# Kernel tuning notes

Measured on AMD Instinct MI355X. Metric: run time of the kernel, lower is better.

The kernel has to match this reference:

```python
import jax, jax.numpy as jnp
import numpy as np

LN_EPS = 1e-5  # torch nn.LayerNorm default

def _layer_norm(x, w, b):
    m = jnp.mean(x, axis=-1, keepdims=True)
    v = jnp.mean(jnp.square(x - m), axis=-1, keepdims=True)
    return (x - m) * jax.lax.rsqrt(v + LN_EPS) * w + b

def setup_inputs() -> dict:
    R, N, D, A = 8, 8192, 2048, 128
    init_scale = 0.01
    key = jax.random.key(0)
    k0, k1, k2 = jax.random.split(key, 3)
    x = jax.random.normal(k0, (N, D), jnp.float32)
    ln_w = jnp.ones((R, D), jnp.float32)              # per-router input LayerNorm weight
    ln_b = jnp.zeros((R, D), jnp.float32)
    router_weights = jax.random.normal(k1, (R, D, A), jnp.float32) * init_scale
    rw_ln_w = jax.random.normal(k2, (R, D), jnp.float32) * init_scale  # weight-LN gamma (init ones*scale in src)
    rw_ln_b = jnp.zeros((R, D), jnp.float32)
    router_bias = jnp.zeros((R, A), jnp.float32)
    return {"x": x, "ln_w": ln_w, "ln_b": ln_b, "router_weights": router_weights,
            "rw_ln_w": rw_ln_w, "rw_ln_b": rw_ln_b, "router_bias": router_bias}

def reference(x, ln_w, ln_b, router_weights, rw_ln_w, rw_ln_b, router_bias):
    # Per-router LayerNorm of shared input x: new_x [R, N, D]
    new_x = jax.vmap(lambda w, b: _layer_norm(x, w, b))(ln_w, ln_b)
    # normalize_router_weights=True: LayerNorm over in_dim of W[i].T, then transpose back
    rw_norm = jax.vmap(lambda W, w, b: _layer_norm(W.T, w, b).T)(router_weights, rw_ln_w, rw_ln_b)  # [R, D, A]
    adapter_logits = jnp.einsum('rnd,rda->rna', new_x, rw_norm) + router_bias[:, None, :]
    adapter_probs = jax.nn.softmax(adapter_logits, axis=-1)
    return new_x, adapter_logits, adapter_probs
```

## Files before the change

kernel.cpp:

```cpp
#include <hip/hip_runtime.h>
#include <hip/hip_bf16.h>
#include <stdint.h>

#define R_ 8
#define N_ 8192
#define D_ 2048
#define A_ 128
#define J_ 1024
#define LN_EPS 1e-5f

typedef __attribute__((ext_vector_type(8))) short bf16x8;
typedef __attribute__((ext_vector_type(4))) float f32x4;

__device__ inline ushort f2bf(float f) {
    union { float f; uint32_t u; } v; v.f = f;
    uint32_t u = v.u;
    return (ushort)((u + 0x7fffu + ((u >> 16) & 1u)) >> 16);
}
__device__ inline float bf2f(ushort u) {
    union { uint32_t u; float f; } v; v.u = ((uint32_t)u) << 16;
    return v.f;
}

__global__ __launch_bounds__(256) void k_prep(
    const float* __restrict__ x,
    const float* __restrict__ W,
    const float* __restrict__ ln_w,
    const float* __restrict__ ln_b,
    const float* __restrict__ rw_w,
    const float* __restrict__ rw_b,
    const float* __restrict__ rbias,
    ushort* __restrict__ xhat,
    ushort* __restrict__ Bt,
    float* __restrict__ cvec)
{
    __shared__ float sm[16];
    const int t = threadIdx.x;

    if (blockIdx.x < N_) {
        const int n = blockIdx.x;
        const float* xr = x + (size_t)n * D_;
        float4 v0 = *(const float4*)(xr + t * 4);
        float4 v1 = *(const float4*)(xr + 1024 + t * 4);
        float s  = v0.x + v0.y + v0.z + v0.w + v1.x + v1.y + v1.z + v1.w;
        float sq = v0.x*v0.x + v0.y*v0.y + v0.z*v0.z + v0.w*v0.w
                 + v1.x*v1.x + v1.y*v1.y + v1.z*v1.z + v1.w*v1.w;
        #pragma unroll
        for (int o = 32; o > 0; o >>= 1) {
            s  += __shfl_xor(s,  o, 64);
            sq += __shfl_xor(sq, o, 64);
        }
        if ((t & 63) == 0) { sm[t >> 6] = s; sm[8 + (t >> 6)] = sq; }
        __syncthreads();
        s  = sm[0] + sm[1] + sm[2] + sm[3];
        sq = sm[8] + sm[9] + sm[10] + sm[11];
        const float mean = s * (1.0f / D_);
        const float var  = sq * (1.0f / D_) - mean * mean;
        const float rstd = rsqrtf(var + LN_EPS);

        ushort4 p0 = make_ushort4(f2bf((v0.x - mean) * rstd), f2bf((v0.y - mean) * rstd),
                                  f2bf((v0.z - mean) * rstd), f2bf((v0.w - mean) * rstd));
        ushort4 p1 = make_ushort4(f2bf((v1.x - mean) * rstd), f2bf((v1.y - mean) * rstd),
                                  f2bf((v1.z - mean) * rstd), f2bf((v1.w - mean) * rstd));
        *(ushort4*)(xhat + (size_t)n * D_ + t * 4)        = p0;
        *(ushort4*)(xhat + (size_t)n * D_ + 1024 + t * 4) = p1;
    } else {
        const int j = blockIdx.x - N_;
        const int r = j >> 7, a = j & 127;
        const float* Wc = W + (size_t)r * D_ * A_ + a;

        float vals[8];
        float s = 0.f, sq = 0.f;
        #pragma unroll
        for (int k = 0; k < 8; ++k) {
            float v = Wc[(size_t)(t + k * 256) * A_];
            vals[k] = v; s += v; sq += v * v;
        }
        #pragma unroll
        for (int o = 32; o > 0; o >>= 1) {
            s  += __shfl_xor(s,  o, 64);
            sq += __shfl_xor(sq, o, 64);
        }
        if ((t & 63) == 0) { sm[t >> 6] = s; sm[8 + (t >> 6)] = sq; }
        __syncthreads();
        s  = sm[0] + sm[1] + sm[2] + sm[3];
        sq = sm[8] + sm[9] + sm[10] + sm[11];
        const float mean = s * (1.0f / D_);
        const float var  = sq * (1.0f / D_) - mean * mean;
        const float rstd = rsqrtf(var + LN_EPS);

        float cp = 0.f;
        #pragma unroll
        for (int k = 0; k < 8; ++k) {
            const int d = t + k * 256;
            const float nv = (vals[k] - mean) * rstd * rw_w[(size_t)r * D_ + d]
                           + rw_b[(size_t)r * D_ + d];
            Bt[(size_t)j * D_ + d] = f2bf(ln_w[(size_t)r * D_ + d] * nv);
            cp += ln_b[(size_t)r * D_ + d] * nv;
        }
        __syncthreads();
        #pragma unroll
        for (int o = 32; o > 0; o >>= 1) cp += __shfl_xor(cp, o, 64);
        if ((t & 63) == 0) sm[t >> 6] = cp;
        __syncthreads();
        if (t == 0) cvec[j] = sm[0] + sm[1] + sm[2] + sm[3] + rbias[(size_t)r * A_ + a];
    }
}

__global__ __launch_bounds__(256) void k_fused(
    const ushort* __restrict__ Xh,
    const ushort* __restrict__ Bt,
    const float* __restrict__ cvec,
    const float* __restrict__ ln_w,
    const float* __restrict__ ln_b,
    float* __restrict__ new_x,
    float* __restrict__ logits,
    float* __restrict__ probs)
{
    __shared__ __attribute__((aligned(16))) ushort As[64 * 32];
    __shared__ __attribute__((aligned(16))) ushort Bs[128 * 32];
    __shared__ __attribute__((aligned(16))) float lwS[D_];
    __shared__ __attribute__((aligned(16))) float lbS[D_];

    const int t    = threadIdx.x;
    const int lane = t & 63;
    const int w    = t >> 6;
    const int r    = blockIdx.x & 7;
    const int mt   = blockIdx.x >> 3;
    const int m0   = mt * 64;
    const int j0   = r * 128;

    #pragma unroll
    for (int i = 0; i < 2; ++i) {
        const int idx = t + i * 256;
        ((float4*)lwS)[idx] = ((const float4*)(ln_w + (size_t)r * D_))[idx];
        ((float4*)lbS)[idx] = ((const float4*)(ln_b + (size_t)r * D_))[idx];
    }

    f32x4 acc[8];
    #pragma unroll
    for (int jf = 0; jf < 8; ++jf) acc[jf] = (f32x4){0.f, 0.f, 0.f, 0.f};

    float* nx_base = new_x + ((size_t)r * N_ + m0) * D_;

    for (int kt = 0; kt < D_ / 32; ++kt) {
        __syncthreads();
        {
            const int row = t >> 2;
            const int kc  = t & 3;
            const ushort* gA = Xh + (size_t)(m0 + row) * D_ + kt * 32 + kc * 8;
            __builtin_amdgcn_global_load_lds(
                (const __attribute__((address_space(1))) void*)gA,
                (__attribute__((address_space(3))) void*)(&As[t * 8]), 16, 0, 0);
        }
        #pragma unroll
        for (int c = 0; c < 2; ++c) {
            const int q   = t + c * 256;
            const int row = q >> 2;
            const int kc  = q & 3;
            const ushort* gB = Bt + (size_t)(j0 + row) * D_ + kt * 32 + kc * 8;
            __builtin_amdgcn_global_load_lds(
                (const __attribute__((address_space(1))) void*)gB,
                (__attribute__((address_space(3))) void*)(&Bs[q * 8]), 16, 0, 0);
        }
        __syncthreads();

        const int kbase = kt * 32;
        #pragma unroll
        for (int c = 0; c < 2; ++c) {
            const int q    = t + c * 256;
            const int row  = q >> 3;
            const int col4 = q & 7;
            const int d    = kbase + col4 * 4;
            const ushort4 hb = *(const ushort4*)(&As[row * 32 + col4 * 4]);
            const float4 lw4 = *(const float4*)(&lwS[d]);
            const float4 lb4 = *(const float4*)(&lbS[d]);
            f32x4 o;
            o[0] = bf2f(hb.x) * lw4.x + lb4.x;
            o[1] = bf2f(hb.y) * lw4.y + lb4.y;
            o[2] = bf2f(hb.z) * lw4.z + lb4.z;
            o[3] = bf2f(hb.w) * lw4.w + lb4.w;
            __builtin_nontemporal_store(o, (f32x4*)(nx_base + (size_t)row * D_ + d));
        }

        const bf16x8 afr = *(const bf16x8*)(&As[(w * 16 + (lane & 15)) * 32
                                                + (lane >> 4) * 8]);
        #pragma unroll
        for (int jf = 0; jf < 8; ++jf) {
            const bf16x8 bfr = *(const bf16x8*)(&Bs[(jf * 16 + (lane & 15)) * 32
                                                    + (lane >> 4) * 8]);
            acc[jf] = __builtin_amdgcn_mfma_f32_16x16x32_bf16(afr, bfr, acc[jf], 0, 0, 0);
        }
    }

    float cv[8];
    #pragma unroll
    for (int jf = 0; jf < 8; ++jf) cv[jf] = cvec[j0 + jf * 16 + (lane & 15)];

    #pragma unroll
    for (int reg = 0; reg < 4; ++reg) {
        const int row = m0 + w * 16 + (lane >> 4) * 4 + reg;
        float v[8], e[8];
        float mx = -3.4e38f;
        #pragma unroll
        for (int jf = 0; jf < 8; ++jf) {
            v[jf] = acc[jf][reg] + cv[jf];
            mx = fmaxf(mx, v[jf]);
        }
        #pragma unroll
        for (int o = 8; o > 0; o >>= 1) mx = fmaxf(mx, __shfl_xor(mx, o, 64));
        float ssum = 0.f;
        #pragma unroll
        for (int jf = 0; jf < 8; ++jf) { e[jf] = __expf(v[jf] - mx); ssum += e[jf]; }
        #pragma unroll
        for (int o = 8; o > 0; o >>= 1) ssum += __shfl_xor(ssum, o, 64);
        const float inv = 1.0f / ssum;
        float* lrow = logits + ((size_t)r * N_ + row) * A_;
        float* prow = probs  + ((size_t)r * N_ + row) * A_;
        #pragma unroll
        for (int jf = 0; jf < 8; ++jf) {
            const int aa = jf * 16 + (lane & 15);
            __builtin_nontemporal_store(v[jf], lrow + aa);
            __builtin_nontemporal_store(e[jf] * inv, prow + aa);
        }
    }
}

extern "C" void kernel_launch(void* const* d_in, const int* in_sizes, int n_in,
                              void* d_out, int out_size, void* d_ws, size_t ws_size,
                              hipStream_t stream)
{
    const float* x     = (const float*)d_in[0];
    const float* ln_w  = (const float*)d_in[1];
    const float* ln_b  = (const float*)d_in[2];
    const float* W     = (const float*)d_in[3];
    const float* rw_w  = (const float*)d_in[4];
    const float* rw_b  = (const float*)d_in[5];
    const float* rbias = (const float*)d_in[6];

    float* out    = (float*)d_out;
    float* new_x  = out;
    float* logits = out + (size_t)R_ * N_ * D_;
    float* probs  = logits + (size_t)R_ * N_ * A_;

    ushort* xhat = (ushort*)d_ws;
    ushort* Btp  = (ushort*)((char*)d_ws + (size_t)N_ * D_ * 2);
    float*  cvec = (float*)((char*)d_ws + (size_t)N_ * D_ * 2 + (size_t)J_ * D_ * 2);

    hipLaunchKernelGGL(k_prep, dim3(N_ + J_), dim3(256), 0, stream,
                       x, W, ln_w, ln_b, rw_w, rw_b, rbias, xhat, Btp, cvec);
    hipLaunchKernelGGL(k_fused, dim3(J_), dim3(256), 0, stream,
                       xhat, Btp, cvec, ln_w, ln_b, new_x, logits, probs);
}
```

Baseline: 191.3 us.

## Double K tile to 64 with XOR-swizzled LDS and bf16 LayerNorm params

Doubles the K step of the fused GEMM loop from 32 to 64, which halves the number of barrier-separated load phases. The A and B tiles are now stored in LDS with an XOR swizzle on the 16-byte chunk index to reduce bank conflicts on the MFMA fragment reads and on the new_x epilogue reads. The per-router LayerNorm weight and bias are kept in LDS as bf16 instead of fp32 to save shared memory. In exchange, new_x loses some precision for arbitrary ln_w/ln_b values, and the larger tiles raise register and LDS pressure per block.

```diff
diff --git a/kernel.cpp b/kernel.cpp
--- a/kernel.cpp
+++ b/kernel.cpp
@@ -117,10 +117,10 @@
     float* __restrict__ logits,
     float* __restrict__ probs)
 {
-    __shared__ __attribute__((aligned(16))) ushort As[64 * 32];
-    __shared__ __attribute__((aligned(16))) ushort Bs[128 * 32];
-    __shared__ __attribute__((aligned(16))) float lwS[D_];
-    __shared__ __attribute__((aligned(16))) float lbS[D_];
+    __shared__ __attribute__((aligned(16))) ushort As[64 * 64];
+    __shared__ __attribute__((aligned(16))) ushort Bs[128 * 64];
+    __shared__ __attribute__((aligned(16))) ushort lwS[D_];
+    __shared__ __attribute__((aligned(16))) ushort lbS[D_];
 
     const int t    = threadIdx.x;
     const int lane = t & 63;
@@ -130,11 +130,15 @@
     const int m0   = mt * 64;
     const int j0   = r * 128;
 
-    #pragma unroll
-    for (int i = 0; i < 2; ++i) {
-        const int idx = t + i * 256;
-        ((float4*)lwS)[idx] = ((const float4*)(ln_w + (size_t)r * D_))[idx];
-        ((float4*)lbS)[idx] = ((const float4*)(ln_b + (size_t)r * D_))[idx];
+    {
+        const float4 wa = ((const float4*)(ln_w + (size_t)r * D_))[2 * t];
+        const float4 wb = ((const float4*)(ln_w + (size_t)r * D_))[2 * t + 1];
+        const float4 ba = ((const float4*)(ln_b + (size_t)r * D_))[2 * t];
+        const float4 bb = ((const float4*)(ln_b + (size_t)r * D_))[2 * t + 1];
+        *(ushort4*)(&lwS[t * 8])     = make_ushort4(f2bf(wa.x), f2bf(wa.y), f2bf(wa.z), f2bf(wa.w));
+        *(ushort4*)(&lwS[t * 8 + 4]) = make_ushort4(f2bf(wb.x), f2bf(wb.y), f2bf(wb.z), f2bf(wb.w));
+        *(ushort4*)(&lbS[t * 8])     = make_ushort4(f2bf(ba.x), f2bf(ba.y), f2bf(ba.z), f2bf(ba.w));
+        *(ushort4*)(&lbS[t * 8 + 4]) = make_ushort4(f2bf(bb.x), f2bf(bb.y), f2bf(bb.z), f2bf(bb.w));
     }
 
     f32x4 acc[8];
@@ -143,53 +147,63 @@
 
     float* nx_base = new_x + ((size_t)r * N_ + m0) * D_;
 
-    for (int kt = 0; kt < D_ / 32; ++kt) {
-        __syncthreads();
-        {
-            const int row = t >> 2;
-            const int kc  = t & 3;
-            const ushort* gA = Xh + (size_t)(m0 + row) * D_ + kt * 32 + kc * 8;
+    for (int kt = 0; kt < 32; ++kt) {
+        __syncthreads();
+        #pragma unroll
+        for (int c = 0; c < 2; ++c) {
+            const int q    = t + c * 256;
+            const int row  = q >> 3;
+            const int slot = q & 7;
+            const int kc   = slot ^ (row & 7);
+            const ushort* gA = Xh + (size_t)(m0 + row) * D_ + kt * 64 + kc * 8;
             __builtin_amdgcn_global_load_lds(
                 (const __attribute__((address_space(1))) void*)gA,
-                (__attribute__((address_space(3))) void*)(&As[t * 8]), 16, 0, 0);
-        }
-        #pragma unroll
-        for (int c = 0; c < 2; ++c) {
-            const int q   = t + c * 256;
-            const int row = q >> 2;
-            const int kc  = q & 3;
-            const ushort* gB = Bt + (size_t)(j0 + row) * D_ + kt * 32 + kc * 8;
+                (__attribute__((address_space(3))) void*)(&As[q * 8]), 16, 0, 0);
+        }
+        #pragma unroll
+        for (int c = 0; c < 4; ++c) {
+            const int q    = t + c * 256;
+            const int row  = q >> 3;
+            const int slot = q & 7;
+            const int kc   = slot ^ (row & 7);
+            const ushort* gB = Bt + (size_t)(j0 + row) * D_ + kt * 64 + kc * 8;
             __builtin_amdgcn_global_load_lds(
                 (const __attribute__((address_space(1))) void*)gB,
                 (__attribute__((address_space(3))) void*)(&Bs[q * 8]), 16, 0, 0);
         }
         __syncthreads();
 
-        const int kbase = kt * 32;
-        #pragma unroll
-        for (int c = 0; c < 2; ++c) {
-            const int q    = t + c * 256;
-            const int row  = q >> 3;
-            const int col4 = q & 7;
-            const int d    = kbase + col4 * 4;
-            const ushort4 hb = *(const ushort4*)(&As[row * 32 + col4 * 4]);
-            const float4 lw4 = *(const float4*)(&lwS[d]);
-            const float4 lb4 = *(const float4*)(&lbS[d]);
+        const int kbase = kt * 64;
+        #pragma unroll
+        for (int c = 0; c < 4; ++c) {
+            const int q     = t + c * 256;
+            const int row   = q >> 4;
+            const int c4    = q & 15;
+            const int pslot = (c4 >> 1) ^ (row & 7);
+            const ushort4 hb = *(const ushort4*)(&As[row * 64 + pslot * 8 + (c4 & 1) * 4]);
+            const int d = kbase + c4 * 4;
+            const ushort4 w4 = *(const ushort4*)(&lwS[d]);
+            const ushort4 b4 = *(const ushort4*)(&lbS[d]);
             f32x4 o;
-            o[0] = bf2f(hb.x) * lw4.x + lb4.x;
-            o[1] = bf2f(hb.y) * lw4.y + lb4.y;
-            o[2] = bf2f(hb.z) * lw4.z + lb4.z;
-            o[3] = bf2f(hb.w) * lw4.w + lb4.w;
+            o[0] = bf2f(hb.x) * bf2f(w4.x) + bf2f(b4.x);
+            o[1] = bf2f(hb.y) * bf2f(w4.y) + bf2f(b4.y);
+            o[2] = bf2f(hb.z) * bf2f(w4.z) + bf2f(b4.z);
+            o[3] = bf2f(hb.w) * bf2f(w4.w) + bf2f(b4.w);
             __builtin_nontemporal_store(o, (f32x4*)(nx_base + (size_t)row * D_ + d));
         }
 
-        const bf16x8 afr = *(const bf16x8*)(&As[(w * 16 + (lane & 15)) * 32
-                                                + (lane >> 4) * 8]);
-        #pragma unroll
-        for (int jf = 0; jf < 8; ++jf) {
-            const bf16x8 bfr = *(const bf16x8*)(&Bs[(jf * 16 + (lane & 15)) * 32
-                                                    + (lane >> 4) * 8]);
-            acc[jf] = __builtin_amdgcn_mfma_f32_16x16x32_bf16(afr, bfr, acc[jf], 0, 0, 0);
+        #pragma unroll
+        for (int kf = 0; kf < 2; ++kf) {
+            const int slot  = (lane >> 4) + 4 * kf;
+            const int pslot = slot ^ (lane & 7);
+            const bf16x8 afr = *(const bf16x8*)(&As[(w * 16 + (lane & 15)) * 64
+                                                    + pslot * 8]);
+            #pragma unroll
+            for (int jf = 0; jf < 8; ++jf) {
+                const bf16x8 bfr = *(const bf16x8*)(&Bs[(jf * 16 + (lane & 15)) * 64
+                                                        + pslot * 8]);
+                acc[jf] = __builtin_amdgcn_mfma_f32_16x16x32_bf16(afr, bfr, acc[jf], 0, 0, 0);
+            }
         }
     }
 
```

Result: faster. 182.8 us (-4.4%).
